# Kernel optimization log

Hardware: AMD Instinct MI355X
Metric: run time of the kernel (lower is better)

The kernel has to match this reference:

```python
import jax, jax.numpy as jnp
import numpy as np

T, B, S, D = 512, 32, 512, 512
EPS = 1e-6  # LayerNorm eps


def _ln(x, g, b):
    m = jnp.mean(x, axis=-1, keepdims=True)
    v = jnp.mean((x - m) ** 2, axis=-1, keepdims=True)
    return g * (x - m) * jax.lax.rsqrt(v + EPS) + b


def setup_inputs() -> dict:
    key = jax.random.key(0)
    ks = jax.random.split(key, 10)
    sc = 1.0 / np.sqrt(D).astype(np.float32)
    return {
        "prev_layer": jax.random.normal(ks[0], (T, B, D), jnp.float32),
        "hidden": jax.random.normal(ks[1], (B, D), jnp.float32),
        "enc_output": jax.random.normal(ks[2], (B, S, D), jnp.float32),
        "memory_length": jax.random.randint(ks[3], (B,), 1, S + 1),
        # nn.Linear weights stored as [in, out] (transposed torch layout)
        "W_in": jax.random.normal(ks[4], (D, 3 * D), jnp.float32) * sc,
        "W_enc": jax.random.normal(ks[5], (D, D), jnp.float32) * sc,
        "W_attn_in": jax.random.normal(ks[6], (D, D), jnp.float32) * sc,
        "W_hidden": jax.random.normal(ks[7], (D, D), jnp.float32) * sc,
        "W_ctx": jax.random.normal(ks[8], (D, D), jnp.float32) * sc,
        # LayerNorm gains/biases (5 LNs)
        "g_pre": jnp.ones((3 * D,), jnp.float32), "b_pre": jnp.zeros((3 * D,), jnp.float32),
        "g_enc": jnp.ones((D,), jnp.float32), "b_enc": jnp.zeros((D,), jnp.float32),
        "g_attn": jnp.ones((D,), jnp.float32), "b_attn": jnp.zeros((D,), jnp.float32),
        "g_h": jnp.ones((D,), jnp.float32), "b_h": jnp.zeros((D,), jnp.float32),
        "g_c": jnp.ones((D,), jnp.float32), "b_c": jnp.zeros((D,), jnp.float32),
    }


def reference(prev_layer, hidden, enc_output, W_in, W_enc, W_attn_in, W_hidden,
              W_ctx, g_pre, b_pre, g_enc, b_enc, g_attn, b_attn, g_h, b_h,
              g_c, b_c, memory_length):
    d = prev_layer.shape[-1]
    sqrt_d = jnp.sqrt(jnp.asarray(d, prev_layer.dtype))
    # dropout is identity in eval mode
    preact = _ln(prev_layer @ W_in, g_pre, b_pre)          # [T,B,3D]
    pctx = _ln(enc_output @ W_enc, g_enc, b_enc)           # [B,S,D]
    z, h_gate, pl_t = jnp.split(preact, 3, axis=-1)
    z = jax.nn.sigmoid(z)
    h_gate = jax.nn.sigmoid(h_gate)

    # SRU-style linear recurrence: s_t = (1-z_t)*s_{t-1} + z_t*pl_t
    def step(h, zp):
        z_t, p_t = zp
        s = (1.0 - z_t) * h + z_t * p_t
        return s, s

    hidden_last, ss = jax.lax.scan(step, hidden, (z, pl_t))  # ss: [T,B,D]

    attn_in = _ln(ss @ W_attn_in, g_attn, b_attn)            # [T,B,D]
    align = jnp.einsum('tbd,bsd->bts', attn_in, pctx)        # [B,T,S]
    mask = jnp.arange(pctx.shape[1])[None, :] < memory_length[:, None]  # [B,S]
    align = jnp.where(mask[:, None, :], align, -jnp.inf)
    av = jax.nn.softmax(align / sqrt_d, axis=-1)             # [B,T,S]
    c = jnp.einsum('bts,bsd->tbd', av, pctx)                 # [T,B,D]
    attn_out = c / sqrt_d

    trans = _ln(ss @ W_hidden, g_h, b_h) + _ln(attn_out @ W_ctx, g_c, b_c)
    out = jnp.tanh(trans)
    out = (1.0 - h_gate) * out + h_gate * prev_layer         # [T,B,D]
    p_attn = jnp.transpose(av, (1, 0, 2))                    # [T,B,S]
    return out, hidden_last, p_attn
```

## Files before the change

### kernel.cpp

```cpp
#include <hip/hip_runtime.h>
#include <hip/hip_bf16.h>
#include <cmath>

#define T_ 512
#define B_ 32
#define S_ 512
#define D_ 512
#define D3_ 1536
#define NCH 16
#define CT (T_ / NCH)
static constexpr float LN_EPS = 1e-6f;
static constexpr float RSQRT_D = 0.044194173824159216f;

typedef __attribute__((ext_vector_type(8))) __bf16 bf16x8;
typedef __attribute__((ext_vector_type(4))) float f32x4;

struct __align__(8) bfx4 { __hip_bfloat16 x, y, z, w; };

__device__ __forceinline__ void g2l16(const void* g, void* l) {
    __builtin_amdgcn_global_load_lds(
        (const __attribute__((address_space(1))) unsigned int*)g,
        (__attribute__((address_space(3))) unsigned int*)l, 16, 0, 0);
}

__device__ __forceinline__ float xr_sum16(float v) {
    v += __shfl_xor(v, 1); v += __shfl_xor(v, 2);
    v += __shfl_xor(v, 4); v += __shfl_xor(v, 8); return v;
}
__device__ __forceinline__ float xr_max16(float v) {
    v = fmaxf(v, __shfl_xor(v, 1)); v = fmaxf(v, __shfl_xor(v, 2));
    v = fmaxf(v, __shfl_xor(v, 4)); v = fmaxf(v, __shfl_xor(v, 8)); return v;
}

__device__ __forceinline__ float sigmoidf_(float x) {
    return 1.f / (1.f + __expf(-x));
}

__global__ __launch_bounds__(256) void gemm_pre(
    const __hip_bfloat16* __restrict__ A,
    const __hip_bfloat16* __restrict__ Bw,
    __hip_bfloat16* __restrict__ preb,
    float2* __restrict__ part)
{
    __shared__ char smem[16384];
    __hip_bfloat16* As = (__hip_bfloat16*)smem;
    __hip_bfloat16* Bs = (__hip_bfloat16*)(smem + 8192);

    const int m0 = blockIdx.y * 128, n0 = blockIdx.x * 128;
    const int tid = threadIdx.x, lane = tid & 63, w = tid >> 6;
    const int wm = (w >> 1) * 64, wn = (w & 1) * 64;
    const int srow = lane >> 2, skB = (lane & 3) * 16;
    const int q = lane >> 4, c = lane & 15;

    f32x4 acc[4][4];
#pragma unroll
    for (int i = 0; i < 4; i++)
#pragma unroll
        for (int j = 0; j < 4; j++) acc[i][j] = (f32x4)(0.0f);

    const char* ga0 = (const char*)(A + (long)(m0 + w * 16 + srow) * 512) + skB;
    const char* ga1 = (const char*)(A + (long)(m0 + (w + 4) * 16 + srow) * 512) + skB;
    const char* gb0 = (const char*)(Bw + (long)(n0 + w * 16 + srow) * 512) + skB;
    const char* gb1 = (const char*)(Bw + (long)(n0 + (w + 4) * 16 + srow) * 512) + skB;
    char* la0 = (char*)As + w * 1024 + lane * 16;
    char* la1 = (char*)As + (w + 4) * 1024 + lane * 16;
    char* lb0 = (char*)Bs + w * 1024 + lane * 16;
    char* lb1 = (char*)Bs + (w + 4) * 1024 + lane * 16;
    const char* Ar = (const char*)As + (wm + c) * 64 + q * 16;
    const char* Br = (const char*)Bs + (wn + c) * 64 + q * 16;

    for (int k0 = 0; k0 < 512; k0 += 32) {
        const long kb = (long)k0 * 2;
        g2l16(ga0 + kb, la0);
        g2l16(ga1 + kb, la1);
        g2l16(gb0 + kb, lb0);
        g2l16(gb1 + kb, lb1);
        __syncthreads();
        bf16x8 af[4], bfr[4];
#pragma unroll
        for (int i = 0; i < 4; i++) {
            af[i] = *(const bf16x8*)(Ar + i * 1024);
            bfr[i] = *(const bf16x8*)(Br + i * 1024);
        }
#pragma unroll
        for (int i = 0; i < 4; i++)
#pragma unroll
            for (int j = 0; j < 4; j++)
                acc[i][j] = __builtin_amdgcn_mfma_f32_16x16x32_bf16(
                    af[i], bfr[j], acc[i][j], 0, 0, 0);
        __syncthreads();
    }

    float2* sred = (float2*)smem;
#pragma unroll
    for (int i = 0; i < 4; i++)
#pragma unroll
        for (int r = 0; r < 4; r++) {
            float s = 0.f, qq = 0.f;
#pragma unroll
            for (int j = 0; j < 4; j++) {
                float v = acc[i][j][r]; s += v; qq += v * v;
            }
            s = xr_sum16(s); qq = xr_sum16(qq);
            if (c == 0) sred[(wm + i * 16 + q * 4 + r) * 2 + (w & 1)] =
                make_float2(s, qq);
        }
    __syncthreads();
    if ((w & 1) == 0 && c == 0) {
#pragma unroll
        for (int i = 0; i < 4; i++)
#pragma unroll
            for (int r = 0; r < 4; r++) {
                int row = wm + i * 16 + q * 4 + r;
                float2 a = sred[row * 2], b2 = sred[row * 2 + 1];
                part[(long)blockIdx.x * 16384 + m0 + row] =
                    make_float2(a.x + b2.x, a.y + b2.y);
            }
    }
    __syncthreads();

    for (int p = 0; p < 2; p++) {
        if ((w >> 1) == p) {
#pragma unroll
            for (int i = 0; i < 4; i++)
#pragma unroll
                for (int j = 0; j < 4; j++)
#pragma unroll
                    for (int r = 0; r < 4; r++) {
                        int row = i * 16 + q * 4 + r;
                        int col = wn + j * 16 + c;
                        ((__hip_bfloat16*)smem)[row * 128 + col] =
                            __float2bfloat16(acc[i][j][r]);
                    }
        }
        __syncthreads();
#pragma unroll
        for (int rnd = 0; rnd < 4; rnd++) {
            int row = rnd * 16 + (tid >> 4);
            int ch = tid & 15;
            uint4 v = *(const uint4*)(smem + row * 256 + ch * 16);
            long grow = m0 + p * 64 + row;
            *(uint4*)((char*)preb + grow * 3072 + (long)n0 * 2 + ch * 16) = v;
        }
        __syncthreads();
    }
}

__device__ __forceinline__ void rows_core32(
    const __hip_bfloat16* A, long lda,
    const __hip_bfloat16* B, long ldb,
    char* smem, f32x4 (&acc)[2][8])
{
    const int tid = threadIdx.x, lane = tid & 63, w = tid >> 6;
#pragma unroll
    for (int m = 0; m < 2; m++)
#pragma unroll
        for (int j = 0; j < 8; j++) acc[m][j] = (f32x4)(0.0f);

    const char* ga = (const char*)(A + (long)(w * 16 + (lane >> 2)) * lda) + (lane & 3) * 16;
    char* la = smem + w * 1024 + lane * 16;
    const char* gb = (const char*)(B + (long)(w * 128 + (lane >> 2)) * ldb) + (lane & 3) * 16;
    char* lb = smem + 2048 + w * 8192 + lane * 16;
    const long ldbB16 = (long)ldb * 32;
    const char* Ar = smem + (lane & 15) * 64 + (lane >> 4) * 16;
    const char* Br = smem + 2048 + (w * 128 + (lane & 15)) * 64 + (lane >> 4) * 16;

    for (int k0 = 0; k0 < 512; k0 += 32) {
        const long kb = (long)k0 * 2;
        if (w < 2) g2l16(ga + kb, la);
#pragma unroll
        for (int s = 0; s < 8; s++) g2l16(gb + kb + s * ldbB16, lb + s * 1024);
        __syncthreads();
        bf16x8 af[2], bfr[8];
#pragma unroll
        for (int m = 0; m < 2; m++) af[m] = *(const bf16x8*)(Ar + m * 1024);
#pragma unroll
        for (int j = 0; j < 8; j++) bfr[j] = *(const bf16x8*)(Br + j * 1024);
#pragma unroll
        for (int m = 0; m < 2; m++)
#pragma unroll
            for (int j = 0; j < 8; j++)
                acc[m][j] = __builtin_amdgcn_mfma_f32_16x16x32_bf16(
                    af[m], bfr[j], acc[m][j], 0, 0, 0);
        __syncthreads();
    }
}

__global__ __launch_bounds__(256, 2) void gemm_ln(
    const __hip_bfloat16* __restrict__ A, long lda,
    const __hip_bfloat16* __restrict__ W,
    const float* __restrict__ g, const float* __restrict__ bb,
    __hip_bfloat16* __restrict__ out)
{
    __shared__ char smem[34816];
    const long m0 = (long)blockIdx.y * 32;
    f32x4 acc[2][8];
    rows_core32(A + m0 * lda, lda, W, 512, smem, acc);

    const int tid = threadIdx.x, lane = tid & 63, w = tid >> 6;
    const int q = lane >> 4, c = lane & 15;
    float2* sred = (float2*)smem;
#pragma unroll
    for (int m = 0; m < 2; m++)
#pragma unroll
        for (int r = 0; r < 4; r++) {
            float s = 0.f, qq = 0.f;
#pragma unroll
            for (int j = 0; j < 8; j++) {
                float v = acc[m][j][r]; s += v; qq += v * v;
            }
            s = xr_sum16(s); qq = xr_sum16(qq);
            if (c == 0) sred[(m * 16 + q * 4 + r) * 4 + w] = make_float2(s, qq);
        }
    __syncthreads();
    float mean[2][4], rstd[2][4];
#pragma unroll
    for (int m = 0; m < 2; m++)
#pragma unroll
        for (int r = 0; r < 4; r++) {
            int row = m * 16 + q * 4 + r;
            float s = 0.f, qq = 0.f;
#pragma unroll
            for (int ww = 0; ww < 4; ww++) {
                float2 t = sred[row * 4 + ww]; s += t.x; qq += t.y;
            }
            float mn = s * (1.f / 512);
            mean[m][r] = mn;
            rstd[m][r] = rsqrtf(qq * (1.f / 512) - mn * mn + LN_EPS);
        }
    __syncthreads();
#pragma unroll
    for (int m = 0; m < 2; m++)
#pragma unroll
        for (int j = 0; j < 8; j++) {
            int col = w * 128 + j * 16 + c;
            float gv = g[col], bv = bb[col];
#pragma unroll
            for (int r = 0; r < 4; r++) {
                int row = m * 16 + q * 4 + r;
                float v = (acc[m][j][r] - mean[m][r]) * rstd[m][r] * gv + bv;
                ((__hip_bfloat16*)smem)[row * 512 + col] = __float2bfloat16(v);
            }
        }
    __syncthreads();
#pragma unroll
    for (int rnd = 0; rnd < 8; rnd++) {
        int row = rnd * 4 + w;
        uint4 v = *(const uint4*)(smem + row * 1024 + lane * 16);
        *(uint4*)((char*)out + (m0 + row) * 1024 + lane * 16) = v;
    }
}

__global__ __launch_bounds__(256, 2) void gemm_attn(
    const __hip_bfloat16* __restrict__ attninb,
    const __hip_bfloat16* __restrict__ pctxb,
    const int* __restrict__ mlen,
    float* __restrict__ pattn, __hip_bfloat16* __restrict__ pattnb)
{
    __shared__ char smem[34816];
    const int b = blockIdx.z;
    const long t0 = (long)blockIdx.y * 32;
    f32x4 acc[2][8];
    rows_core32(attninb + (long)b * 512 + t0 * 16384, 16384,
                pctxb + (long)b * 262144, 512, smem, acc);

    const int tid = threadIdx.x, lane = tid & 63, w = tid >> 6;
    const int q = lane >> 4, c = lane & 15;
    const int len = mlen[b];
    float* sred = (float*)smem;

#pragma unroll
    for (int m = 0; m < 2; m++)
#pragma unroll
        for (int r = 0; r < 4; r++) {
            float mx = -INFINITY;
#pragma unroll
            for (int j = 0; j < 8; j++) {
                int col = w * 128 + j * 16 + c;
                float v = acc[m][j][r] * RSQRT_D;
                acc[m][j][r] = v;
                if (col < len) mx = fmaxf(mx, v);
            }
            mx = xr_max16(mx);
            if (c == 0) sred[(m * 16 + q * 4 + r) * 4 + w] = mx;
        }
    __syncthreads();
    float rmax[2][4];
#pragma unroll
    for (int m = 0; m < 2; m++)
#pragma unroll
        for (int r = 0; r < 4; r++) {
            int row = m * 16 + q * 4 + r;
            rmax[m][r] = fmaxf(fmaxf(sred[row * 4], sred[row * 4 + 1]),
                               fmaxf(sred[row * 4 + 2], sred[row * 4 + 3]));
        }
    __syncthreads();
#pragma unroll
    for (int m = 0; m < 2; m++)
#pragma unroll
        for (int r = 0; r < 4; r++) {
            float s = 0.f;
#pragma unroll
            for (int j = 0; j < 8; j++) {
                int col = w * 128 + j * 16 + c;
                float e = (col < len) ? __expf(acc[m][j][r] - rmax[m][r]) : 0.f;
                acc[m][j][r] = e; s += e;
            }
            s = xr_sum16(s);
            if (c == 0) sred[(m * 16 + q * 4 + r) * 4 + w] = s;
        }
    __syncthreads();
    float rinv[2][4];
#pragma unroll
    for (int m = 0; m < 2; m++)
#pragma unroll
        for (int r = 0; r < 4; r++) {
            int row = m * 16 + q * 4 + r;
            rinv[m][r] = 1.f / (sred[row * 4] + sred[row * 4 + 1] +
                                sred[row * 4 + 2] + sred[row * 4 + 3]);
        }
    __syncthreads();

#pragma unroll
    for (int m = 0; m < 2; m++)
#pragma unroll
        for (int j = 0; j < 8; j++)
#pragma unroll
            for (int r = 0; r < 4; r++) {
                int row = m * 16 + q * 4 + r;
                int col = w * 128 + j * 16 + c;
                float p = acc[m][j][r] * rinv[m][r];
                acc[m][j][r] = p;
                pattn[((t0 + row) * 32 + b) * 512 + col] = p;
                ((__hip_bfloat16*)smem)[row * 512 + col] = __float2bfloat16(p);
            }
    __syncthreads();
#pragma unroll
    for (int rnd = 0; rnd < 8; rnd++) {
        int row = rnd * 4 + w;
        uint4 v = *(const uint4*)(smem + row * 1024 + lane * 16);
        *(uint4*)((char*)pattnb + ((t0 + row) * 32 + b) * 1024 + lane * 16) = v;
    }
}

__global__ __launch_bounds__(256, 2) void gemm_av(
    const __hip_bfloat16* __restrict__ pattnb,
    const __hip_bfloat16* __restrict__ pctxT,
    __hip_bfloat16* __restrict__ attnoutb)
{
    __shared__ char smem[34816];
    const int b = blockIdx.z;
    const long t0 = (long)blockIdx.y * 32;
    f32x4 acc[2][8];
    rows_core32(pattnb + (long)b * 512 + t0 * 16384, 16384,
                pctxT + (long)b * 262144, 512, smem, acc);

    const int tid = threadIdx.x, lane = tid & 63, w = tid >> 6;
    const int q = lane >> 4, c = lane & 15;
#pragma unroll
    for (int m = 0; m < 2; m++)
#pragma unroll
        for (int j = 0; j < 8; j++)
#pragma unroll
            for (int r = 0; r < 4; r++) {
                int row = m * 16 + q * 4 + r;
                int col = w * 128 + j * 16 + c;
                ((__hip_bfloat16*)smem)[row * 512 + col] =
                    __float2bfloat16(acc[m][j][r] * RSQRT_D);
            }
    __syncthreads();
#pragma unroll
    for (int rnd = 0; rnd < 8; rnd++) {
        int row = rnd * 4 + w;
        uint4 v = *(const uint4*)(smem + row * 1024 + lane * 16);
        *(uint4*)((char*)attnoutb + ((t0 + row) * 32 + b) * 1024 + lane * 16) = v;
    }
}

__global__ __launch_bounds__(256, 2) void gemm_fin(
    const __hip_bfloat16* __restrict__ attnoutb,
    const __hip_bfloat16* __restrict__ Wc,
    const __hip_bfloat16* __restrict__ h1n,
    const __hip_bfloat16* __restrict__ preb,
    const float2* __restrict__ stats,
    const float* __restrict__ g_c, const float* __restrict__ b_c,
    const float* __restrict__ g_pre, const float* __restrict__ b_pre,
    const float* __restrict__ prev, float* __restrict__ out)
{
    __shared__ char smem[34816];
    const long m0 = (long)blockIdx.y * 32;
    f32x4 acc[2][8];
    rows_core32(attnoutb + m0 * 512, 512, Wc, 512, smem, acc);

    const int tid = threadIdx.x, lane = tid & 63, w = tid >> 6;
    const int q = lane >> 4, c = lane & 15;
    float2* sred = (float2*)smem;
#pragma unroll
    for (int m = 0; m < 2; m++)
#pragma unroll
        for (int r = 0; r < 4; r++) {
            float s = 0.f, qq = 0.f;
#pragma unroll
            for (int j = 0; j < 8; j++) {
                float v = acc[m][j][r]; s += v; qq += v * v;
            }
            s = xr_sum16(s); qq = xr_sum16(qq);
            if (c == 0) sred[(m * 16 + q * 4 + r) * 4 + w] = make_float2(s, qq);
        }
    __syncthreads();
#pragma unroll
    for (int m = 0; m < 2; m++)
#pragma unroll
        for (int r = 0; r < 4; r++) {
            int row = m * 16 + q * 4 + r;
            float s = 0.f, qq = 0.f;
#pragma unroll
            for (int ww = 0; ww < 4; ww++) {
                float2 t = sred[row * 4 + ww]; s += t.x; qq += t.y;
            }
            float mn = s * (1.f / 512);
            float rs = rsqrtf(qq * (1.f / 512) - mn * mn + LN_EPS);
            long rowg = m0 + row;
            float2 sh = stats[rowg];
#pragma unroll
            for (int j = 0; j < 8; j++) {
                int col = w * 128 + j * 16 + c;
                float t2 = (acc[m][j][r] - mn) * rs * g_c[col] + b_c[col];
                float t1 = __bfloat162float(h1n[rowg * 512 + col]);
                float hraw = __bfloat162float(preb[rowg * 1536 + 512 + col]);
                float hg = sigmoidf_((hraw - sh.x) * sh.y * g_pre[512 + col] +
                                     b_pre[512 + col]);
                float pv = prev[rowg * 512 + col];
                float o = tanhf(t1 + t2);
                out[rowg * 512 + col] = (1.f - hg) * o + hg * pv;
            }
        }
}

__global__ __launch_bounds__(256) void cvt4(
    const float* __restrict__ x, __hip_bfloat16* __restrict__ y, int n4)
{
    int i = blockIdx.x * 256 + threadIdx.x;
    if (i >= n4) return;
    float4 v = ((const float4*)x)[i];
    bfx4 o;
    o.x = __float2bfloat16(v.x); o.y = __float2bfloat16(v.y);
    o.z = __float2bfloat16(v.z); o.w = __float2bfloat16(v.w);
    ((bfx4*)y)[i] = o;
}

__global__ __launch_bounds__(256) void wtrans(
    const float* __restrict__ w0, const float* __restrict__ w1,
    const float* __restrict__ w2, const float* __restrict__ w3,
    const float* __restrict__ w4, __hip_bfloat16* __restrict__ WT)
{
    int z = blockIdx.z;
    const float* W; long off; int N;
    if (z == 0)      { W = w0; off = 0;                N = 1536; }
    else if (z == 1) { W = w1; off = 786432;           N = 512; }
    else if (z == 2) { W = w2; off = 786432 + 262144;  N = 512; }
    else if (z == 3) { W = w3; off = 786432 + 524288;  N = 512; }
    else             { W = w4; off = 786432 + 786432;  N = 512; }
    int n0 = blockIdx.x * 32, k0 = blockIdx.y * 32;
    if (n0 >= N) return;
    __shared__ float t[32][33];
    int tx = threadIdx.x & 31, ty = threadIdx.x >> 5;
#pragma unroll
    for (int i = 0; i < 4; i++)
        t[ty + i * 8][tx] = W[(long)(k0 + ty + i * 8) * N + n0 + tx];
    __syncthreads();
    __hip_bfloat16* O = WT + off;
#pragma unroll
    for (int i = 0; i < 4; i++)
        O[(long)(n0 + ty + i * 8) * 512 + k0 + tx] =
            __float2bfloat16(t[tx][ty + i * 8]);
}

__global__ __launch_bounds__(256) void ptrans(
    const __hip_bfloat16* __restrict__ src, __hip_bfloat16* __restrict__ dst)
{
    long boff = (long)blockIdx.z * (S_ * D_);
    int d0 = blockIdx.x * 32, s0 = blockIdx.y * 32;
    __shared__ __hip_bfloat16 t[32][34];
    int tx = threadIdx.x & 31, ty = threadIdx.x >> 5;
#pragma unroll
    for (int i = 0; i < 4; i++)
        t[ty + i * 8][tx] = src[boff + (long)(s0 + ty + i * 8) * D_ + d0 + tx];
    __syncthreads();
#pragma unroll
    for (int i = 0; i < 4; i++)
        dst[boff + (long)(d0 + ty + i * 8) * S_ + s0 + tx] = t[tx][ty + i * 8];
}

__global__ __launch_bounds__(256) void stats_fin(
    const float2* __restrict__ part, float2* __restrict__ stats)
{
    int r = blockIdx.x * 256 + threadIdx.x;
    float s = 0.f, qq = 0.f;
#pragma unroll
    for (int cb = 0; cb < 12; cb++) {
        float2 v = part[(long)cb * 16384 + r]; s += v.x; qq += v.y;
    }
    float m = s * (1.f / 1536);
    float rs = rsqrtf(qq * (1.f / 1536) - m * m + LN_EPS);
    stats[r] = make_float2(m, rs);
}

__global__ __launch_bounds__(256) void scan_part1(
    const __hip_bfloat16* __restrict__ preb, const float2* __restrict__ stats,
    const float* __restrict__ gpre, const float* __restrict__ bpre,
    float* __restrict__ Ap, float* __restrict__ Bp)
{
    int idx = blockIdx.x * 256 + threadIdx.x;
    int b = idx >> 9, d = idx & 511;
    int ch = blockIdx.y;
    float gz = gpre[d], bz = bpre[d];
    float gp = gpre[1024 + d], bpv = bpre[1024 + d];
    float A = 1.f, s = 0.f;
    for (int t = ch * CT; t < (ch + 1) * CT; t++) {
        long row = (long)t * 32 + b;
        float2 st = stats[row];
        float zr = __bfloat162float(preb[row * 1536 + d]);
        float pr = __bfloat162float(preb[row * 1536 + 1024 + d]);
        float z = sigmoidf_((zr - st.x) * st.y * gz + bz);
        float pl = (pr - st.x) * st.y * gp + bpv;
        float a = 1.f - z;
        A *= a;
        s = a * s + z * pl;
    }
    Ap[ch * 16384 + idx] = A;
    Bp[ch * 16384 + idx] = s;
}

__global__ __launch_bounds__(256) void scan_part2(
    const float* __restrict__ Ap, const float* __restrict__ Bp,
    const float* __restrict__ h0, float* __restrict__ sin_,
    float* __restrict__ hlast)
{
    int idx = blockIdx.x * 256 + threadIdx.x;
    float s = h0[idx];
    for (int ch = 0; ch < NCH; ch++) {
        sin_[ch * 16384 + idx] = s;
        s = Ap[ch * 16384 + idx] * s + Bp[ch * 16384 + idx];
    }
    hlast[idx] = s;
}

__global__ __launch_bounds__(256) void scan_part3(
    const __hip_bfloat16* __restrict__ preb, const float2* __restrict__ stats,
    const float* __restrict__ gpre, const float* __restrict__ bpre,
    const float* __restrict__ sin_, __hip_bfloat16* __restrict__ ssb)
{
    int idx = blockIdx.x * 256 + threadIdx.x;
    int b = idx >> 9, d = idx & 511;
    int ch = blockIdx.y;
    float gz = gpre[d], bz = bpre[d];
    float gp = gpre[1024 + d], bpv = bpre[1024 + d];
    float s = sin_[ch * 16384 + idx];
    for (int t = ch * CT; t < (ch + 1) * CT; t++) {
        long row = (long)t * 32 + b;
        float2 st = stats[row];
        float zr = __bfloat162float(preb[row * 1536 + d]);
        float pr = __bfloat162float(preb[row * 1536 + 1024 + d]);
        float z = sigmoidf_((zr - st.x) * st.y * gz + bz);
        float pl = (pr - st.x) * st.y * gp + bpv;
        s += z * (pl - s);
        ssb[(long)t * 16384 + idx] = __float2bfloat16(s);
    }
}

extern "C" void kernel_launch(void* const* d_in, const int* in_sizes, int n_in,
                              void* d_out, int out_size, void* d_ws, size_t ws_size,
                              hipStream_t stream) {
    const float* prev  = (const float*)d_in[0];
    const float* hid0  = (const float*)d_in[1];
    const float* enc   = (const float*)d_in[2];
    const int*   mlen  = (const int*)  d_in[3];
    const float* W_in  = (const float*)d_in[4];
    const float* W_enc = (const float*)d_in[5];
    const float* W_att = (const float*)d_in[6];
    const float* W_hid = (const float*)d_in[7];
    const float* W_ctx = (const float*)d_in[8];
    const float* g_pre = (const float*)d_in[9];
    const float* b_pre = (const float*)d_in[10];
    const float* g_enc = (const float*)d_in[11];
    const float* b_enc = (const float*)d_in[12];
    const float* g_att = (const float*)d_in[13];
    const float* b_att = (const float*)d_in[14];
    const float* g_h   = (const float*)d_in[15];
    const float* b_h   = (const float*)d_in[16];
    const float* g_c   = (const float*)d_in[17];
    const float* b_c   = (const float*)d_in[18];

    float* out   = (float*)d_out;
    float* hlast = out + (long)T_ * B_ * D_;
    float* pattn = hlast + (long)B_ * D_;

    char* ws = (char*)d_ws;
    __hip_bfloat16* preb    = (__hip_bfloat16*)(ws);
    __hip_bfloat16* WT      = (__hip_bfloat16*)(ws + 50331648);
    __hip_bfloat16* prevb   = (__hip_bfloat16*)(ws + 54525952);
    __hip_bfloat16* encb    = (__hip_bfloat16*)(ws + 71303168);
    __hip_bfloat16* pctxb   = (__hip_bfloat16*)(ws + 88080384);
    __hip_bfloat16* pctxT   = (__hip_bfloat16*)(ws + 104857600);
    __hip_bfloat16* ssb     = (__hip_bfloat16*)(ws + 121634816);
    __hip_bfloat16* attninb = (__hip_bfloat16*)(ws + 138412032);
    __hip_bfloat16* pattnb  = (__hip_bfloat16*)(ws + 155189248);
    __hip_bfloat16* attnoutb= (__hip_bfloat16*)(ws + 171966464);
    __hip_bfloat16* h1n     = (__hip_bfloat16*)(ws + 188743680);
    float2* part            = (float2*)(ws + 205520896);
    float2* stats           = (float2*)(ws + 207093760);
    float* scanA            = (float*)(ws + 207224832);
    float* scanB            = (float*)(ws + 208273408);
    float* sinb             = (float*)(ws + 209321984);

    const __hip_bfloat16* W_encT = WT + 786432;
    const __hip_bfloat16* W_attT = WT + 786432 + 262144;
    const __hip_bfloat16* W_hidT = WT + 786432 + 524288;
    const __hip_bfloat16* W_ctxT = WT + 786432 + 786432;

    dim3 blk(256);

    cvt4<<<8192, blk, 0, stream>>>(prev, prevb, 2097152);
    cvt4<<<8192, blk, 0, stream>>>(enc, encb, 2097152);
    wtrans<<<dim3(48, 16, 5), blk, 0, stream>>>(W_in, W_enc, W_att, W_hid,
                                                W_ctx, WT);

    gemm_pre<<<dim3(12, 128), blk, 0, stream>>>(prevb, WT, preb, part);
    stats_fin<<<64, blk, 0, stream>>>(part, stats);

    scan_part1<<<dim3(64, NCH), blk, 0, stream>>>(preb, stats, g_pre, b_pre,
                                                  scanA, scanB);
    scan_part2<<<64, blk, 0, stream>>>(scanA, scanB, hid0, sinb, hlast);
    scan_part3<<<dim3(64, NCH), blk, 0, stream>>>(preb, stats, g_pre, b_pre,
                                                  sinb, ssb);

    gemm_ln<<<dim3(1, 512), blk, 0, stream>>>(encb, 512, W_encT, g_enc, b_enc,
                                              pctxb);
    ptrans<<<dim3(16, 16, 32), blk, 0, stream>>>(pctxb, pctxT);

    gemm_ln<<<dim3(1, 512), blk, 0, stream>>>(ssb, 512, W_attT, g_att, b_att,
                                              attninb);

    gemm_attn<<<dim3(1, 16, 32), blk, 0, stream>>>(attninb, pctxb, mlen,
                                                   pattn, pattnb);

    gemm_av<<<dim3(1, 16, 32), blk, 0, stream>>>(pattnb, pctxT, attnoutb);

    gemm_ln<<<dim3(1, 512), blk, 0, stream>>>(ssb, 512, W_hidT, g_h, b_h, h1n);

    gemm_fin<<<dim3(1, 512), blk, 0, stream>>>(attnoutb, W_ctxT, h1n, preb,
                                               stats, g_c, b_c, g_pre, b_pre,
                                               prev, out);
}
```

Measured before the change: 465.3 us.

## Double-buffer LDS tiles in rows_core32 and vectorize the final gated epilogue

The shared K-loop of the row GEMMs now prefetches the next 32-wide K slice into a second LDS buffer while MFMAs run on the current one. This roughly doubles static LDS per block, which may limit blocks per CU. The gemm_fin epilogue first stages the LayerNorm'd context term in LDS, then processes rows with coalesced float4 and ushort4 loads of h1n, preb and prev. It also swaps tanhf and the division-based sigmoid for fast exp/fdividef forms, cutting strided scalar global accesses and transcendental cost at a small accuracy risk.

After: 444.4 us. -4.5%, faster.

```diff
diff --git a/kernel.cpp b/kernel.cpp
--- a/kernel.cpp
+++ b/kernel.cpp
@@ -34,6 +34,16 @@
 
 __device__ __forceinline__ float sigmoidf_(float x) {
     return 1.f / (1.f + __expf(-x));
+}
+__device__ __forceinline__ float sigmoid_fast(float x) {
+    return __fdividef(1.f, 1.f + __expf(-x));
+}
+__device__ __forceinline__ float tanh_fast(float x) {
+    return 1.f - __fdividef(2.f, __expf(2.f * x) + 1.f);
+}
+__device__ __forceinline__ float bfu(unsigned short u) {
+    unsigned int v = ((unsigned int)u) << 16;
+    return __uint_as_float(v);
 }
 
 __global__ __launch_bounds__(256) void gemm_pre(
@@ -146,6 +156,7 @@
     }
 }
 
+#define RC_BUF 34816
 __device__ __forceinline__ void rows_core32(
     const __hip_bfloat16* A, long lda,
     const __hip_bfloat16* B, long ldb,
@@ -165,17 +176,27 @@
     const char* Ar = smem + (lane & 15) * 64 + (lane >> 4) * 16;
     const char* Br = smem + 2048 + (w * 128 + (lane & 15)) * 64 + (lane >> 4) * 16;
 
-    for (int k0 = 0; k0 < 512; k0 += 32) {
-        const long kb = (long)k0 * 2;
-        if (w < 2) g2l16(ga + kb, la);
-#pragma unroll
-        for (int s = 0; s < 8; s++) g2l16(gb + kb + s * ldbB16, lb + s * 1024);
-        __syncthreads();
+    if (w < 2) g2l16(ga, la);
+#pragma unroll
+    for (int s = 0; s < 8; s++) g2l16(gb + s * ldbB16, lb + s * 1024);
+    __syncthreads();
+
+#pragma unroll
+    for (int kk = 0; kk < 16; kk++) {
+        const int cb = (kk & 1) * RC_BUF;
+        const int nb = ((kk & 1) ^ 1) * RC_BUF;
+        if (kk < 15) {
+            const long kb = (long)(kk + 1) * 64;
+            if (w < 2) g2l16(ga + kb, la + nb);
+#pragma unroll
+            for (int s = 0; s < 8; s++)
+                g2l16(gb + kb + s * ldbB16, lb + nb + s * 1024);
+        }
         bf16x8 af[2], bfr[8];
 #pragma unroll
-        for (int m = 0; m < 2; m++) af[m] = *(const bf16x8*)(Ar + m * 1024);
-#pragma unroll
-        for (int j = 0; j < 8; j++) bfr[j] = *(const bf16x8*)(Br + j * 1024);
+        for (int m = 0; m < 2; m++) af[m] = *(const bf16x8*)(Ar + cb + m * 1024);
+#pragma unroll
+        for (int j = 0; j < 8; j++) bfr[j] = *(const bf16x8*)(Br + cb + j * 1024);
 #pragma unroll
         for (int m = 0; m < 2; m++)
 #pragma unroll
@@ -192,7 +213,7 @@
     const float* __restrict__ g, const float* __restrict__ bb,
     __hip_bfloat16* __restrict__ out)
 {
-    __shared__ char smem[34816];
+    __shared__ char smem[69632];
     const long m0 = (long)blockIdx.y * 32;
     f32x4 acc[2][8];
     rows_core32(A + m0 * lda, lda, W, 512, smem, acc);
@@ -257,7 +278,7 @@
     const int* __restrict__ mlen,
     float* __restrict__ pattn, __hip_bfloat16* __restrict__ pattnb)
 {
-    __shared__ char smem[34816];
+    __shared__ char smem[69632];
     const int b = blockIdx.z;
     const long t0 = (long)blockIdx.y * 32;
     f32x4 acc[2][8];
@@ -348,7 +369,7 @@
     const __hip_bfloat16* __restrict__ pctxT,
     __hip_bfloat16* __restrict__ attnoutb)
 {
-    __shared__ char smem[34816];
+    __shared__ char smem[69632];
     const int b = blockIdx.z;
     const long t0 = (long)blockIdx.y * 32;
     f32x4 acc[2][8];
@@ -387,7 +408,7 @@
     const float* __restrict__ g_pre, const float* __restrict__ b_pre,
     const float* __restrict__ prev, float* __restrict__ out)
 {
-    __shared__ char smem[34816];
+    __shared__ char smem[69632];
     const long m0 = (long)blockIdx.y * 32;
     f32x4 acc[2][8];
     rows_core32(attnoutb + m0 * 512, 512, Wc, 512, smem, acc);
@@ -408,6 +429,7 @@
             if (c == 0) sred[(m * 16 + q * 4 + r) * 4 + w] = make_float2(s, qq);
         }
     __syncthreads();
+    float mean[2][4], rstd[2][4];
 #pragma unroll
     for (int m = 0; m < 2; m++)
 #pragma unroll
@@ -419,22 +441,53 @@
                 float2 t = sred[row * 4 + ww]; s += t.x; qq += t.y;
             }
             float mn = s * (1.f / 512);
-            float rs = rsqrtf(qq * (1.f / 512) - mn * mn + LN_EPS);
-            long rowg = m0 + row;
-            float2 sh = stats[rowg];
-#pragma unroll
-            for (int j = 0; j < 8; j++) {
-                int col = w * 128 + j * 16 + c;
-                float t2 = (acc[m][j][r] - mn) * rs * g_c[col] + b_c[col];
-                float t1 = __bfloat162float(h1n[rowg * 512 + col]);
-                float hraw = __bfloat162float(preb[rowg * 1536 + 512 + col]);
-                float hg = sigmoidf_((hraw - sh.x) * sh.y * g_pre[512 + col] +
-                                     b_pre[512 + col]);
-                float pv = prev[rowg * 512 + col];
-                float o = tanhf(t1 + t2);
-                out[rowg * 512 + col] = (1.f - hg) * o + hg * pv;
-            }
-        }
+            mean[m][r] = mn;
+            rstd[m][r] = rsqrtf(qq * (1.f / 512) - mn * mn + LN_EPS);
+        }
+    __syncthreads();
+
+    float* t2s = (float*)smem;
+#pragma unroll
+    for (int m = 0; m < 2; m++)
+#pragma unroll
+        for (int j = 0; j < 8; j++) {
+            int col = w * 128 + j * 16 + c;
+            float gv = g_c[col], bv = b_c[col];
+#pragma unroll
+            for (int r = 0; r < 4; r++) {
+                int row = m * 16 + q * 4 + r;
+                t2s[row * 512 + col] =
+                    (acc[m][j][r] - mean[m][r]) * rstd[m][r] * gv + bv;
+            }
+        }
+    __syncthreads();
+
+#pragma unroll
+    for (int ch = 0; ch < 16; ch++) {
+        int f4 = ch * 256 + tid;
+        int row = f4 >> 7;
+        long rowg = m0 + row;
+        int col = (f4 & 127) * 4;
+        float4 t2 = ((const float4*)t2s)[f4];
+        ushort4 h1 = *(const ushort4*)((const char*)h1n + rowg * 1024 + col * 2);
+        ushort4 hr = *(const ushort4*)((const char*)preb + rowg * 3072 + 1024 + col * 2);
+        float4 pv = *(const float4*)(prev + rowg * 512 + col);
+        float4 gp = *(const float4*)(g_pre + 512 + col);
+        float4 bp = *(const float4*)(b_pre + 512 + col);
+        float2 sh = stats[rowg];
+        auto fuse = [&](unsigned short h1u, unsigned short hru, float t2v,
+                        float pvv, float gpv, float bpv) -> float {
+            float hg = sigmoid_fast((bfu(hru) - sh.x) * sh.y * gpv + bpv);
+            float th = tanh_fast(bfu(h1u) + t2v);
+            return (1.f - hg) * th + hg * pvv;
+        };
+        float4 o;
+        o.x = fuse(h1.x, hr.x, t2.x, pv.x, gp.x, bp.x);
+        o.y = fuse(h1.y, hr.y, t2.y, pv.y, gp.y, bp.y);
+        o.z = fuse(h1.z, hr.z, t2.z, pv.z, gp.z, bp.z);
+        o.w = fuse(h1.w, hr.w, t2.w, pv.w, gp.w, bp.w);
+        *(float4*)(out + rowg * 512 + col) = o;
+    }
 }
 
 __global__ __launch_bounds__(256) void cvt4(
```
